# Kernel tuning notes

Measured on AMD Instinct MI355X. Metric: run time of the kernel, lower is better.

The kernel has to match this reference:

```python
import jax, jax.numpy as jnp
import numpy as np

N_NODES = 50000
N_EDGES = 1000000
F_IN, HID, N_CLS, HEADS = 128, 16, 40, 8
NEG_SLOPE = 0.2


def setup_inputs() -> dict:
    key = jax.random.key(0)
    ks = jax.random.split(key, 12)
    x = jax.random.normal(ks[0], (N_NODES, F_IN), dtype=jnp.float32)
    edge_index = jax.random.randint(ks[1], (2, N_EDGES), 0, N_NODES, dtype=jnp.int32)
    s1 = 1.0 / np.sqrt(F_IN)
    s2 = 1.0 / np.sqrt(HID)
    return {
        "x": x,
        "edge_index": edge_index,
        # conv1: heads=8, out=HID, concat=False (mean over heads)
        "W1": jax.random.normal(ks[2], (F_IN, HEADS * HID), dtype=jnp.float32) * s1,
        "att_src1": jax.random.normal(ks[3], (HEADS, HID), dtype=jnp.float32) * s2,
        "att_dst1": jax.random.normal(ks[4], (HEADS, HID), dtype=jnp.float32) * s2,
        "b1": jnp.zeros((HID,), dtype=jnp.float32),
        # conv2: heads=1, out=N_CLS
        "W2": jax.random.normal(ks[5], (HID, N_CLS), dtype=jnp.float32) * s2,
        "att_src2": jax.random.normal(ks[6], (1, N_CLS), dtype=jnp.float32),
        "att_dst2": jax.random.normal(ks[7], (1, N_CLS), dtype=jnp.float32),
        "b2": jnp.zeros((N_CLS,), dtype=jnp.float32),
    }


def _gat_conv(x, src, dst, W, att_src, att_dst, num_nodes):
    """One GATConv (PyG semantics, eval mode). Returns [N, H, C]."""
    H, C = att_src.shape
    h = (x @ W).reshape(-1, H, C)                       # [N, H, C]
    a_s = (h * att_src[None]).sum(-1)                   # [N, H]
    a_d = (h * att_dst[None]).sum(-1)                   # [N, H]
    e = jax.nn.leaky_relu(a_s[src] + a_d[dst], NEG_SLOPE)  # [E, H]
    # segment softmax over edges grouped by destination node
    m = jax.ops.segment_max(e, dst, num_segments=num_nodes)     # [N, H]
    ex = jnp.exp(e - m[dst])
    denom = jax.ops.segment_sum(ex, dst, num_segments=num_nodes)
    alpha = ex / (denom[dst] + 1e-16)                   # [E, H]
    msg = h[src] * alpha[:, :, None]                    # [E, H, C]
    return jax.ops.segment_sum(msg, dst, num_segments=num_nodes)  # [N, H, C]


def reference(x, edge_index, W1, att_src1, att_dst1, b1, W2, att_src2, att_dst2, b2):
    n = x.shape[0]
    loops = jnp.arange(n, dtype=edge_index.dtype)
    src = jnp.concatenate([edge_index[0], loops])
    dst = jnp.concatenate([edge_index[1], loops])

    # conv1: concat=False -> mean over heads, then bias; then ELU
    h1 = _gat_conv(x, src, dst, W1, att_src1, att_dst1, n).mean(axis=1) + b1
    h1 = jax.nn.elu(h1)
    # dropout is identity in eval mode

    # conv2: heads=1, concat (trivial) -> squeeze head dim, add bias
    h2 = _gat_conv(h1, src, dst, W2, att_src2, att_dst2, n)[:, 0, :] + b2
    return jax.nn.log_softmax(h2, axis=1)
```

## Files before the change

### kernel.cpp

```cpp
#include <hip/hip_runtime.h>
#include <hip/hip_fp16.h>
#include <math.h>

#define N_NODES 50000
#define N_EDGES 1000000
#define F_IN 128
#define HID 16
#define N_CLS 40
#define HEADS 8
#define ET (N_EDGES + N_NODES)
#define XB ((N_NODES + 63) / 64)
#define HB ((ET + 255) / 256)
#define NSCB ((N_NODES + 255) / 256)

__device__ __forceinline__ void fma4(float4& acc, float s, const float4& v) {
  acc.x += s * v.x;
  acc.y += s * v.y;
  acc.z += s * v.z;
  acc.w += s * v.w;
}

__device__ __forceinline__ float dot4(float4 a, float4 b) {
  return a.x * b.x + a.y * b.y + a.z * b.z + a.w * b.w;
}

__device__ __forceinline__ unsigned encf(float f) {
  unsigned b = __float_as_uint(f);
  return (b & 0x80000000u) ? ~b : (b | 0x80000000u);
}
__device__ __forceinline__ float decf(unsigned k) {
  unsigned b = (k & 0x80000000u) ? (k ^ 0x80000000u) : ~k;
  return __uint_as_float(b);
}


__global__ __launch_bounds__(256, 4) void k_xform1(
    const float* __restrict__ x, const float* __restrict__ W1,
    const float* __restrict__ att_s, const float* __restrict__ att_d,
    const int* __restrict__ ei, int* __restrict__ deg, int* __restrict__ epos,
    __half* __restrict__ h1, float* __restrict__ as1, float* __restrict__ ad1,
    unsigned* __restrict__ enc1) {
  if (blockIdx.x >= XB) {
    int i = (blockIdx.x - XB) * 256 + threadIdx.x;
    if (i < ET) {
      int dd = (i < N_EDGES) ? ei[N_EDGES + i] : (i - N_EDGES);
      epos[i] = atomicAdd(&deg[dd], 1);
    }
    return;
  }
  __shared__ float4 xlds[64 * 9];
  __shared__ float4 wlds[32 * 33];
  __shared__ unsigned encl[8];
  int t = threadIdx.x;
  if (t < 8) encl[t] = 0u;
  int tx = t & 15, ty = t >> 4;
  int base = blockIdx.x * 64;
  const float4* x4 = (const float4*)x;
  const float4* W4 = (const float4*)W1;

  float4 accA[4], accB[4];
#pragma unroll
  for (int n = 0; n < 4; n++) {
    accA[n] = {0.f, 0.f, 0.f, 0.f};
    accB[n] = {0.f, 0.f, 0.f, 0.f};
  }
  int n0 = ty * 4;

  for (int kb = 0; kb < 4; kb++) {
    __syncthreads();
    {
      int i = t;
      int n = i >> 3, q = i & 7;
      int gn = base + n;
      float4 v = {0.f, 0.f, 0.f, 0.f};
      if (gn < N_NODES) v = x4[(size_t)gn * 32 + kb * 8 + q];
      xlds[n * 9 + q] = v;
      i += 256;
      n = i >> 3; q = i & 7;
      gn = base + n;
      float4 v2 = {0.f, 0.f, 0.f, 0.f};
      if (gn < N_NODES) v2 = x4[(size_t)gn * 32 + kb * 8 + q];
      xlds[n * 9 + q] = v2;
    }
#pragma unroll
    for (int u = 0; u < 4; u++) {
      int i = t + u * 256;
      int r = i >> 5, q = i & 31;
      wlds[r * 33 + q] = W4[(size_t)(kb * 32 + r) * 32 + q];
    }
    __syncthreads();
#pragma unroll
    for (int kk = 0; kk < 8; kk++) {
      float4 xv0 = xlds[(n0 + 0) * 9 + kk];
      float4 xv1 = xlds[(n0 + 1) * 9 + kk];
      float4 xv2 = xlds[(n0 + 2) * 9 + kk];
      float4 xv3 = xlds[(n0 + 3) * 9 + kk];
#pragma unroll
      for (int j = 0; j < 4; j++) {
        float4 wA = wlds[(kk * 4 + j) * 33 + tx];
        float4 wB = wlds[(kk * 4 + j) * 33 + tx + 16];
        float s0 = (j == 0) ? xv0.x : (j == 1) ? xv0.y : (j == 2) ? xv0.z : xv0.w;
        float s1 = (j == 0) ? xv1.x : (j == 1) ? xv1.y : (j == 2) ? xv1.z : xv1.w;
        float s2 = (j == 0) ? xv2.x : (j == 1) ? xv2.y : (j == 2) ? xv2.z : xv2.w;
        float s3 = (j == 0) ? xv3.x : (j == 1) ? xv3.y : (j == 2) ? xv3.z : xv3.w;
        fma4(accA[0], s0, wA); fma4(accB[0], s0, wB);
        fma4(accA[1], s1, wA); fma4(accB[1], s1, wB);
        fma4(accA[2], s2, wA); fma4(accB[2], s2, wB);
        fma4(accA[3], s3, wA); fma4(accB[3], s3, wB);
      }
    }
  }

  int c4 = tx * 4;
  float4 asA = *(const float4*)(att_s + c4);
  float4 asB = *(const float4*)(att_s + 64 + c4);
  float4 adA = *(const float4*)(att_d + c4);
  float4 adB = *(const float4*)(att_d + 64 + c4);
  float mxA = -1e30f, mxB = -1e30f;
#pragma unroll
  for (int n = 0; n < 4; n++) {
    int gn = base + n0 + n;
    float psA = dot4(accA[n], asA);
    float psB = dot4(accB[n], asB);
    float pdA = dot4(accA[n], adA);
    float pdB = dot4(accB[n], adB);
    psA += __shfl_xor(psA, 1); psA += __shfl_xor(psA, 2);
    psB += __shfl_xor(psB, 1); psB += __shfl_xor(psB, 2);
    pdA += __shfl_xor(pdA, 1); pdA += __shfl_xor(pdA, 2);
    pdB += __shfl_xor(pdB, 1); pdB += __shfl_xor(pdB, 2);
    if (gn < N_NODES) {
      uint2 pkA, pkB;
      __half2* phA = (__half2*)&pkA;
      __half2* phB = (__half2*)&pkB;
      phA[0] = __floats2half2_rn(accA[n].x, accA[n].y);
      phA[1] = __floats2half2_rn(accA[n].z, accA[n].w);
      phB[0] = __floats2half2_rn(accB[n].x, accB[n].y);
      phB[1] = __floats2half2_rn(accB[n].z, accB[n].w);
      *(uint2*)(h1 + (size_t)gn * 128 + c4) = pkA;
      *(uint2*)(h1 + (size_t)gn * 128 + 64 + c4) = pkB;
      mxA = fmaxf(mxA, psA);
      mxB = fmaxf(mxB, psB);
      if ((tx & 3) == 0) {
        as1[gn * 8 + (tx >> 2)] = psA;
        as1[gn * 8 + 4 + (tx >> 2)] = psB;
        ad1[gn * 8 + (tx >> 2)] = pdA;
        ad1[gn * 8 + 4 + (tx >> 2)] = pdB;
      }
    }
  }
  if ((tx & 3) == 0) {
    atomicMax(&encl[tx >> 2], encf(mxA));
    atomicMax(&encl[4 + (tx >> 2)], encf(mxB));
  }
  __syncthreads();
  if (t < 8) atomicMax(&enc1[t], encl[t]);
}


__global__ __launch_bounds__(256) void k_scanA(const int* __restrict__ deg,
                                               int* __restrict__ bsum) {
  int i = blockIdx.x * 256 + threadIdx.x;
  int v = (i < N_NODES) ? deg[i] : 0;
#pragma unroll
  for (int off = 32; off; off >>= 1) v += __shfl_xor(v, off);
  __shared__ int ws[4];
  if ((threadIdx.x & 63) == 0) ws[threadIdx.x >> 6] = v;
  __syncthreads();
  if (threadIdx.x == 0) bsum[blockIdx.x] = ws[0] + ws[1] + ws[2] + ws[3];
}

__global__ __launch_bounds__(256) void k_scanB(const int* __restrict__ bsum,
                                               int* __restrict__ boff,
                                               int* __restrict__ start,
                                               const unsigned* __restrict__ enc1,
                                               float* __restrict__ fmax1) {
  __shared__ int s[256];
  int t = threadIdx.x;
  int v0 = (t < NSCB) ? bsum[t] : 0;
  s[t] = v0;
  __syncthreads();
  for (int off = 1; off < 256; off <<= 1) {
    int v = (t >= off) ? s[t - off] : 0;
    __syncthreads();
    s[t] += v;
    __syncthreads();
  }
  boff[t] = s[t] - v0;
  if (t == 0) start[N_NODES] = ET;
  if (t < 8) fmax1[t] = decf(enc1[t]);
}

__global__ __launch_bounds__(256) void k_scanC(const int* __restrict__ deg,
                                               const int* __restrict__ boff,
                                               int* __restrict__ start) {
  __shared__ int s[256];
  int t = threadIdx.x;
  int i = blockIdx.x * 256 + t;
  int v0 = (i < N_NODES) ? deg[i] : 0;
  s[t] = v0;
  __syncthreads();
  for (int off = 1; off < 256; off <<= 1) {
    int v = (t >= off) ? s[t - off] : 0;
    __syncthreads();
    s[t] += v;
    __syncthreads();
  }
  if (i < N_NODES) start[i] = boff[blockIdx.x] + s[t] - v0;
}

__global__ void k_scatter(const int* __restrict__ ei, const int* __restrict__ start,
                          const int* __restrict__ epos, int* __restrict__ esrc) {
  int i = blockIdx.x * blockDim.x + threadIdx.x;
  if (i >= ET) return;
  int s, d;
  if (i < N_EDGES) { s = ei[i]; d = ei[N_EDGES + i]; }
  else { s = i - N_EDGES; d = s; }
  esrc[start[d] + epos[i]] = s;
}


__global__ __launch_bounds__(256) void k_agg1(
    const __half* __restrict__ h1, const float* __restrict__ as1,
    const float* __restrict__ ad1, const int* __restrict__ start,
    const int* __restrict__ esrc, const float* __restrict__ b1,
    const float* __restrict__ W2, const float* __restrict__ att_s2,
    const float* __restrict__ att_d2, const float* __restrict__ fmax1,
    __half* __restrict__ h2, float* __restrict__ as2, float* __restrict__ ad2) {
  __shared__ __align__(16) __half2 p_t[4][4 * 164];
  __shared__ __align__(16) int s_off[4][4][20];
  __shared__ float w2s[16 * 40];
  int t = threadIdx.x;
  for (int i = t; i < 640; i += 256) w2s[i] = W2[i];
  __syncthreads();

  int wave = t >> 6, lane = t & 63;
  int g = lane >> 4, li = lane & 15;
  int d = blockIdx.x * 16 + wave * 4 + g;
  int s0 = start[d];
  int deg = start[d + 1] - s0;

  int dm = deg;
  dm = max(dm, __shfl_xor(dm, 16));
  dm = max(dm, __shfl_xor(dm, 32));

  float4 av0 = *(const float4*)(ad1 + d * 8);
  float4 av1 = *(const float4*)(ad1 + d * 8 + 4);
  float ad_[8] = {av0.x, av0.y, av0.z, av0.w, av1.x, av1.y, av1.z, av1.w};
  float c_[8];
#pragma unroll
  for (int h = 0; h < 8; h++) {
    float e = fmax1[h] + ad_[h];
    c_[h] = e > 0.f ? e : 0.2f * e;
  }

  float den = 0.f;
  float accf[8];
#pragma unroll
  for (int k = 0; k < 8; k++) accf[k] = 0.f;

  int hsel = li >> 1;
  const char* h1l = (const char*)(h1 + li * 8);
  __half2* ptw = &p_t[wave][g * 164];
  const int* so = &s_off[wave][g][0];

  for (int be = 0; be < dm; be += 16) {
    int cnt = deg - be;
    bool act = li < cnt;
    int s = 0;
    if (act) s = esrc[s0 + be + li];
    s_off[wave][g][li] = act ? (s << 8) : 0;
    float4 p0 = {0.f, 0.f, 0.f, 0.f}, p1 = {0.f, 0.f, 0.f, 0.f};
    if (act) {
      p0 = *(const float4*)(as1 + (size_t)s * 8);
      p1 = *(const float4*)(as1 + (size_t)s * 8 + 4);
    }
    float ev[8] = {p0.x, p0.y, p0.z, p0.w, p1.x, p1.y, p1.z, p1.w};
#pragma unroll
    for (int h = 0; h < 8; h++) {
      float v = ev[h] + ad_[h];
      v = v > 0.f ? v : 0.2f * v;
      float pv = act ? __expf(v - c_[h]) : 0.f;
      __half hp = __float2half(pv);
      ptw[h * 20 + li] = __half2{hp, hp};
    }
    asm volatile("s_waitcnt lgkmcnt(0)" ::: "memory");

    int cm = min(dm - be, 16);
    const __half2* pt = ptw + hsel * 20;
    __half2 a0 = __floats2half2_rn(0.f, 0.f);
    __half2 a1 = __floats2half2_rn(0.f, 0.f);
    __half2 a2 = __floats2half2_rn(0.f, 0.f);
    __half2 a3 = __floats2half2_rn(0.f, 0.f);
    for (int e = 0; e < cm; e += 8) {
      int4 s4 = *(const int4*)&so[e];
      int4 s8 = *(const int4*)&so[e + 4];
      uint4 pwA = *(const uint4*)&pt[e];
      uint4 pwB = *(const uint4*)&pt[e + 4];
      const __half2* ppA = (const __half2*)&pwA;
      const __half2* ppB = (const __half2*)&pwB;
      uint4 hA = *(const uint4*)(h1l + (unsigned)s4.x);
      uint4 hB = *(const uint4*)(h1l + (unsigned)s4.y);
      uint4 hC = *(const uint4*)(h1l + (unsigned)s4.z);
      uint4 hD = *(const uint4*)(h1l + (unsigned)s4.w);
      uint4 hE = *(const uint4*)(h1l + (unsigned)s8.x);
      uint4 hF = *(const uint4*)(h1l + (unsigned)s8.y);
      uint4 hG = *(const uint4*)(h1l + (unsigned)s8.z);
      uint4 hH = *(const uint4*)(h1l + (unsigned)s8.w);
      const __half2* vA = (const __half2*)&hA;
      const __half2* vB = (const __half2*)&hB;
      const __half2* vC = (const __half2*)&hC;
      const __half2* vD = (const __half2*)&hD;
      const __half2* vE = (const __half2*)&hE;
      const __half2* vF = (const __half2*)&hF;
      const __half2* vG = (const __half2*)&hG;
      const __half2* vH = (const __half2*)&hH;
      a0 = __hfma2(vA[0], ppA[0], a0); a1 = __hfma2(vA[1], ppA[0], a1);
      a2 = __hfma2(vA[2], ppA[0], a2); a3 = __hfma2(vA[3], ppA[0], a3);
      a0 = __hfma2(vB[0], ppA[1], a0); a1 = __hfma2(vB[1], ppA[1], a1);
      a2 = __hfma2(vB[2], ppA[1], a2); a3 = __hfma2(vB[3], ppA[1], a3);
      a0 = __hfma2(vC[0], ppA[2], a0); a1 = __hfma2(vC[1], ppA[2], a1);
      a2 = __hfma2(vC[2], ppA[2], a2); a3 = __hfma2(vC[3], ppA[2], a3);
      a0 = __hfma2(vD[0], ppA[3], a0); a1 = __hfma2(vD[1], ppA[3], a1);
      a2 = __hfma2(vD[2], ppA[3], a2); a3 = __hfma2(vD[3], ppA[3], a3);
      a0 = __hfma2(vE[0], ppB[0], a0); a1 = __hfma2(vE[1], ppB[0], a1);
      a2 = __hfma2(vE[2], ppB[0], a2); a3 = __hfma2(vE[3], ppB[0], a3);
      a0 = __hfma2(vF[0], ppB[1], a0); a1 = __hfma2(vF[1], ppB[1], a1);
      a2 = __hfma2(vF[2], ppB[1], a2); a3 = __hfma2(vF[3], ppB[1], a3);
      a0 = __hfma2(vG[0], ppB[2], a0); a1 = __hfma2(vG[1], ppB[2], a1);
      a2 = __hfma2(vG[2], ppB[2], a2); a3 = __hfma2(vG[3], ppB[2], a3);
      a0 = __hfma2(vH[0], ppB[3], a0); a1 = __hfma2(vH[1], ppB[3], a1);
      a2 = __hfma2(vH[2], ppB[3], a2); a3 = __hfma2(vH[3], ppB[3], a3);
      den += __low2float(ppA[0]) + __low2float(ppA[1]) +
             __low2float(ppA[2]) + __low2float(ppA[3]) +
             __low2float(ppB[0]) + __low2float(ppB[1]) +
             __low2float(ppB[2]) + __low2float(ppB[3]);
    }
    float2 f0 = __half22float2(a0), f1 = __half22float2(a1);
    float2 f2 = __half22float2(a2), f3 = __half22float2(a3);
    accf[0] += f0.x; accf[1] += f0.y; accf[2] += f1.x; accf[3] += f1.y;
    accf[4] += f2.x; accf[5] += f2.y; accf[6] += f3.x; accf[7] += f3.y;
    asm volatile("s_waitcnt lgkmcnt(0)" ::: "memory");
  }

  float sc = 0.125f / den;
#pragma unroll
  for (int k = 0; k < 8; k++) accf[k] *= sc;
#pragma unroll
  for (int off = 2; off <= 8; off <<= 1) {
#pragma unroll
    for (int k = 0; k < 8; k++) accf[k] += __shfl_xor(accf[k], off);
  }
  int jb = (li & 1) * 8;
  float4 b1a = *(const float4*)(b1 + jb);
  float4 b1b = *(const float4*)(b1 + jb + 4);
  float bv[8] = {b1a.x, b1a.y, b1a.z, b1a.w, b1b.x, b1b.y, b1b.z, b1b.w};
  float r[8];
#pragma unroll
  for (int k = 0; k < 8; k++) {
    float v = accf[k] + bv[k];
    r[k] = v > 0.f ? v : __expf(v) - 1.f;
  }
  float ro[8];
#pragma unroll
  for (int k = 0; k < 8; k++) ro[k] = __shfl_xor(r[k], 1);

  float o0 = 0.f, o1 = 0.f, o2 = 0.f;
  bool has2 = li < 8;
#pragma unroll
  for (int k = 0; k < 16; k++) {
    float rk;
    if (k < 8) rk = (li & 1) ? ro[k] : r[k];
    else       rk = (li & 1) ? r[k - 8] : ro[k - 8];
    o0 = fmaf(rk, w2s[k * 40 + li], o0);
    o1 = fmaf(rk, w2s[k * 40 + li + 16], o1);
    if (has2) o2 = fmaf(rk, w2s[k * 40 + li + 32], o2);
  }
  __half* h2r = h2 + d * 40;
  h2r[li] = __float2half(o0);
  h2r[li + 16] = __float2half(o1);
  if (has2) h2r[li + 32] = __float2half(o2);

  float sv = o0 * att_s2[li] + o1 * att_s2[li + 16];
  float dv = o0 * att_d2[li] + o1 * att_d2[li + 16];
  if (has2) {
    sv = fmaf(o2, att_s2[li + 32], sv);
    dv = fmaf(o2, att_d2[li + 32], dv);
  }
#pragma unroll
  for (int off = 1; off <= 8; off <<= 1) {
    sv += __shfl_xor(sv, off);
    dv += __shfl_xor(dv, off);
  }
  if (li == 0) { as2[d] = sv; ad2[d] = dv; }
}


__global__ __launch_bounds__(256) void k_maxas2(const float* __restrict__ as2,
                                                unsigned* __restrict__ enc) {
  int t = blockIdx.x * 256 + threadIdx.x;
  float mx = -1e30f;
  for (int r = t; r < N_NODES; r += 16384) mx = fmaxf(mx, as2[r]);
#pragma unroll
  for (int off = 32; off; off >>= 1) mx = fmaxf(mx, __shfl_xor(mx, off));
  if ((threadIdx.x & 63) == 0) atomicMax(enc, encf(mx));
}


__global__ __launch_bounds__(256) void k_agg2(
    const __half* __restrict__ h2, const float* __restrict__ as2,
    const float* __restrict__ ad2, const int* __restrict__ start,
    const int* __restrict__ esrc, const float* __restrict__ b2,
    const unsigned* __restrict__ as2maxEnc, float* __restrict__ out) {
  __shared__ __align__(16) float p_l[4][64];
  __shared__ __align__(16) int s_l[4][64];
  int wave = threadIdx.x >> 6, lane = threadIdx.x & 63;
  int d = blockIdx.x * 4 + wave;
  if (d >= N_NODES) return;
  int s0 = start[d];
  int deg = start[d + 1] - s0;
  float adv = ad2[d];
  float cm = decf(as2maxEnc[0]) + adv;
  cm = cm > 0.f ? cm : 0.2f * cm;

  int cp = lane % 20;
  int es = lane / 20;
  const char* h2b = (const char*)h2 + cp * 4;

  float den = 0.f, acc0 = 0.f, acc1 = 0.f;
  for (int be = 0; be < deg; be += 64) {
    int cnt = min(64, deg - be);
    if (lane < cnt) {
      int s = esrc[s0 + be + lane];
      s_l[wave][lane] = s * 80;
      float e = as2[s] + adv;
      e = e > 0.f ? e : 0.2f * e;
      float p = __expf(e - cm);
      den += p;
      p_l[wave][lane] = p;
    }
    asm volatile("s_waitcnt lgkmcnt(0)" ::: "memory");
    if (es < 3) {
      int i = 0;
      for (; i + 5 < cnt; i += 6) {
        int eA = i + es, eB = i + 3 + es;
        int sbA = s_l[wave][eA], sbB = s_l[wave][eB];
        float pA = p_l[wave][eA], pB = p_l[wave][eB];
        __half2 hvA = *(const __half2*)(h2b + (unsigned)sbA);
        __half2 hvB = *(const __half2*)(h2b + (unsigned)sbB);
        acc0 = fmaf(__half2float(hvA.x), pA, acc0);
        acc1 = fmaf(__half2float(hvA.y), pA, acc1);
        acc0 = fmaf(__half2float(hvB.x), pB, acc0);
        acc1 = fmaf(__half2float(hvB.y), pB, acc1);
      }
      for (; i < cnt; i += 3) {
        int e = i + es;
        if (e < cnt) {
          int sb = s_l[wave][e];
          float p = p_l[wave][e];
          __half2 hv = *(const __half2*)(h2b + (unsigned)sb);
          acc0 = fmaf(__half2float(hv.x), p, acc0);
          acc1 = fmaf(__half2float(hv.y), p, acc1);
        }
      }
    }
    asm volatile("s_waitcnt lgkmcnt(0)" ::: "memory");
  }
#pragma unroll
  for (int off = 32; off; off >>= 1) den += __shfl_xor(den, off);
  float iv = 1.f / den;

  acc0 += __shfl(acc0, lane + 20) + __shfl(acc0, lane + 40);
  acc1 += __shfl(acc1, lane + 20) + __shfl(acc1, lane + 40);
  float va = __shfl(acc0, lane >> 1);
  float vb = __shfl(acc1, lane >> 1);
  float v = (lane & 1) ? vb : va;
  v = (lane < N_CLS) ? v * iv + b2[lane] : -1e30f;

  float mx = v;
#pragma unroll
  for (int off = 32; off; off >>= 1) mx = fmaxf(mx, __shfl_xor(mx, off));
  float ex = (lane < N_CLS) ? __expf(v - mx) : 0.f;
  float sm = ex;
#pragma unroll
  for (int off = 32; off; off >>= 1) sm += __shfl_xor(sm, off);
  float lse = logf(sm);
  if (lane < N_CLS) out[d * N_CLS + lane] = (v - mx) - lse;
}


extern "C" void kernel_launch(void* const* d_in, const int* in_sizes, int n_in,
                              void* d_out, int out_size, void* d_ws, size_t ws_size,
                              hipStream_t stream) {
  const float* x    = (const float*)d_in[0];
  const int*   ei   = (const int*)d_in[1];
  const float* W1   = (const float*)d_in[2];
  const float* as1w = (const float*)d_in[3];
  const float* ad1w = (const float*)d_in[4];
  const float* b1   = (const float*)d_in[5];
  const float* W2   = (const float*)d_in[6];
  const float* as2w = (const float*)d_in[7];
  const float* ad2w = (const float*)d_in[8];
  const float* b2   = (const float*)d_in[9];
  float* out = (float*)d_out;

  char* ws = (char*)d_ws;
  size_t off = 0;
  auto alloc = [&](size_t bytes) -> void* {
    void* p = ws + off;
    off += (bytes + 255) & ~(size_t)255;
    return p;
  };
  __half* h1   = (__half*)alloc((size_t)N_NODES * 128 * 2);
  float* as1   = (float*)alloc((size_t)N_NODES * 8 * 4);
  float* ad1   = (float*)alloc((size_t)N_NODES * 8 * 4);
  __half* h2   = (__half*)alloc((size_t)N_NODES * 40 * 2);
  float* as2   = (float*)alloc((size_t)N_NODES * 4);
  float* ad2   = (float*)alloc((size_t)N_NODES * 4);
  size_t zbytes = (size_t)N_NODES * 4 + 256;
  int* deg     = (int*)alloc(zbytes);
  unsigned* maxenc = (unsigned*)(deg + N_NODES);
  int* start   = (int*)alloc((size_t)(N_NODES + 1) * 4);
  int* esrc    = (int*)alloc((size_t)ET * 4);
  int* epos    = (int*)alloc((size_t)ET * 4);
  int* bsum    = (int*)alloc((size_t)NSCB * 4);
  int* boff    = (int*)alloc(256 * 4);
  float* fmax1 = (float*)alloc(32);

  (void)hipMemsetAsync(deg, 0, zbytes, stream);

  k_xform1<<<XB + HB, 256, 0, stream>>>(x, W1, as1w, ad1w, ei, deg, epos,
                                        h1, as1, ad1, maxenc);
  k_scanA<<<NSCB, 256, 0, stream>>>(deg, bsum);
  k_scanB<<<1, 256, 0, stream>>>(bsum, boff, start, maxenc, fmax1);
  k_scanC<<<NSCB, 256, 0, stream>>>(deg, boff, start);
  k_scatter<<<HB, 256, 0, stream>>>(ei, start, epos, esrc);

  k_agg1<<<N_NODES / 16, 256, 0, stream>>>(h1, as1, ad1, start, esrc, b1,
                                           W2, as2w, ad2w, fmax1,
                                           h2, as2, ad2);
  k_maxas2<<<64, 256, 0, stream>>>(as2, maxenc + 8);
  k_agg2<<<(N_NODES + 3) / 4, 256, 0, stream>>>(h2, as2, ad2, start, esrc, b2,
                                                maxenc + 8, out);
}
```

Measured before the change: 172.0 us.

## Use fp16 MFMA for first-layer feature transform with swizzled LDS tiles

Rewrites the x@W1 projection to convert x and W1 to fp16 in swizzled shared memory and compute with 16x16x32 MFMA instructions instead of scalar FP32 FMAs. Attention logits are reduced via cross-lane shuffles from the MFMA accumulator layout. This trades input precision (fp16 inputs) and larger LDS use, which may lower occupancy, for higher matrix throughput. Output stores become per-element half writes.

New measurement: 186.9 us. 1.09x slower.

```diff
diff --git a/kernel.cpp b/kernel.cpp
--- a/kernel.cpp
+++ b/kernel.cpp
@@ -13,16 +13,8 @@
 #define HB ((ET + 255) / 256)
 #define NSCB ((N_NODES + 255) / 256)
 
-__device__ __forceinline__ void fma4(float4& acc, float s, const float4& v) {
-  acc.x += s * v.x;
-  acc.y += s * v.y;
-  acc.z += s * v.z;
-  acc.w += s * v.w;
-}
-
-__device__ __forceinline__ float dot4(float4 a, float4 b) {
-  return a.x * b.x + a.y * b.y + a.z * b.z + a.w * b.w;
-}
+typedef __attribute__((ext_vector_type(8))) _Float16 f16x8;
+typedef __attribute__((ext_vector_type(4))) float f32x4;
 
 __device__ __forceinline__ unsigned encf(float f) {
   unsigned b = __float_as_uint(f);
@@ -34,7 +26,7 @@
 }
 
 
-__global__ __launch_bounds__(256, 4) void k_xform1(
+__global__ __launch_bounds__(256) void k_xform1(
     const float* __restrict__ x, const float* __restrict__ W1,
     const float* __restrict__ att_s, const float* __restrict__ att_d,
     const int* __restrict__ ei, int* __restrict__ deg, int* __restrict__ epos,
@@ -48,109 +40,107 @@
     }
     return;
   }
-  __shared__ float4 xlds[64 * 9];
-  __shared__ float4 wlds[32 * 33];
+  __shared__ __half xl[64 * 128];
+  __shared__ __half wt[128 * 128];
   __shared__ unsigned encl[8];
   int t = threadIdx.x;
   if (t < 8) encl[t] = 0u;
-  int tx = t & 15, ty = t >> 4;
   int base = blockIdx.x * 64;
   const float4* x4 = (const float4*)x;
   const float4* W4 = (const float4*)W1;
 
-  float4 accA[4], accB[4];
-#pragma unroll
-  for (int n = 0; n < 4; n++) {
-    accA[n] = {0.f, 0.f, 0.f, 0.f};
-    accB[n] = {0.f, 0.f, 0.f, 0.f};
-  }
-  int n0 = ty * 4;
-
+#pragma unroll
+  for (int u = 0; u < 8; u++) {
+    int i = t + u * 256;
+    int n = i >> 5, q = i & 31;
+    int gn = base + n;
+    float4 v = {0.f, 0.f, 0.f, 0.f};
+    if (gn < N_NODES) v = x4[(size_t)gn * 32 + q];
+    uint2 pk;
+    __half2* ph = (__half2*)&pk;
+    ph[0] = __floats2half2_rn(v.x, v.y);
+    ph[1] = __floats2half2_rn(v.z, v.w);
+    unsigned byte = (unsigned)(n * 256 + q * 8) ^ ((n & 7) << 4);
+    *(uint2*)((char*)xl + byte) = pk;
+  }
+#pragma unroll
+  for (int u = 0; u < 4; u++) {
+    int i = t + u * 256;
+    int kt = i >> 5, ct = i & 31;
+    int k0 = kt * 4;
+    float4 r0 = W4[(size_t)(k0 + 0) * 32 + ct];
+    float4 r1 = W4[(size_t)(k0 + 1) * 32 + ct];
+    float4 r2 = W4[(size_t)(k0 + 2) * 32 + ct];
+    float4 r3 = W4[(size_t)(k0 + 3) * 32 + ct];
+    int chb = ct * 4;
+    uint2 pk;
+    __half2* ph = (__half2*)&pk;
+    ph[0] = __floats2half2_rn(r0.x, r1.x); ph[1] = __floats2half2_rn(r2.x, r3.x);
+    *(uint2*)((char*)wt + (((unsigned)((chb + 0) * 256 + k0 * 2)) ^ (((chb + 0) & 7) << 4))) = pk;
+    ph[0] = __floats2half2_rn(r0.y, r1.y); ph[1] = __floats2half2_rn(r2.y, r3.y);
+    *(uint2*)((char*)wt + (((unsigned)((chb + 1) * 256 + k0 * 2)) ^ (((chb + 1) & 7) << 4))) = pk;
+    ph[0] = __floats2half2_rn(r0.z, r1.z); ph[1] = __floats2half2_rn(r2.z, r3.z);
+    *(uint2*)((char*)wt + (((unsigned)((chb + 2) * 256 + k0 * 2)) ^ (((chb + 2) & 7) << 4))) = pk;
+    ph[0] = __floats2half2_rn(r0.w, r1.w); ph[1] = __floats2half2_rn(r2.w, r3.w);
+    *(uint2*)((char*)wt + (((unsigned)((chb + 3) * 256 + k0 * 2)) ^ (((chb + 3) & 7) << 4))) = pk;
+  }
+  __syncthreads();
+
+  int l = t & 63, wv = t >> 6;
+  int lm = l & 15, lh = l >> 4;
+  int n0 = wv * 16;
+  int node = n0 + lm;
+  bool wvalid = (base + n0) < N_NODES;
+
+  f32x4 acc[8];
+#pragma unroll
+  for (int f = 0; f < 8; f++) acc[f] = (f32x4){0.f, 0.f, 0.f, 0.f};
+
+#pragma unroll
   for (int kb = 0; kb < 4; kb++) {
-    __syncthreads();
-    {
-      int i = t;
-      int n = i >> 3, q = i & 7;
-      int gn = base + n;
-      float4 v = {0.f, 0.f, 0.f, 0.f};
-      if (gn < N_NODES) v = x4[(size_t)gn * 32 + kb * 8 + q];
-      xlds[n * 9 + q] = v;
-      i += 256;
-      n = i >> 3; q = i & 7;
-      gn = base + n;
-      float4 v2 = {0.f, 0.f, 0.f, 0.f};
-      if (gn < N_NODES) v2 = x4[(size_t)gn * 32 + kb * 8 + q];
-      xlds[n * 9 + q] = v2;
-    }
-#pragma unroll
-    for (int u = 0; u < 4; u++) {
-      int i = t + u * 256;
-      int r = i >> 5, q = i & 31;
-      wlds[r * 33 + q] = W4[(size_t)(kb * 32 + r) * 32 + q];
-    }
-    __syncthreads();
-#pragma unroll
-    for (int kk = 0; kk < 8; kk++) {
-      float4 xv0 = xlds[(n0 + 0) * 9 + kk];
-      float4 xv1 = xlds[(n0 + 1) * 9 + kk];
-      float4 xv2 = xlds[(n0 + 2) * 9 + kk];
-      float4 xv3 = xlds[(n0 + 3) * 9 + kk];
-#pragma unroll
-      for (int j = 0; j < 4; j++) {
-        float4 wA = wlds[(kk * 4 + j) * 33 + tx];
-        float4 wB = wlds[(kk * 4 + j) * 33 + tx + 16];
-        float s0 = (j == 0) ? xv0.x : (j == 1) ? xv0.y : (j == 2) ? xv0.z : xv0.w;
-        float s1 = (j == 0) ? xv1.x : (j == 1) ? xv1.y : (j == 2) ? xv1.z : xv1.w;
-        float s2 = (j == 0) ? xv2.x : (j == 1) ? xv2.y : (j == 2) ? xv2.z : xv2.w;
-        float s3 = (j == 0) ? xv3.x : (j == 1) ? xv3.y : (j == 2) ? xv3.z : xv3.w;
-        fma4(accA[0], s0, wA); fma4(accB[0], s0, wB);
-        fma4(accA[1], s1, wA); fma4(accB[1], s1, wB);
-        fma4(accA[2], s2, wA); fma4(accB[2], s2, wB);
-        fma4(accA[3], s3, wA); fma4(accB[3], s3, wB);
+    int kbase = kb * 32 + lh * 8;
+    unsigned ab = ((unsigned)(node * 256 + kbase * 2)) ^ ((node & 7) << 4);
+    f16x8 af = *(const f16x8*)((const char*)xl + ab);
+#pragma unroll
+    for (int f = 0; f < 8; f++) {
+      int ch = f * 16 + lm;
+      unsigned bb = ((unsigned)(ch * 256 + kbase * 2)) ^ ((ch & 7) << 4);
+      f16x8 bf = *(const f16x8*)((const char*)wt + bb);
+      acc[f] = __builtin_amdgcn_mfma_f32_16x16x32_f16(af, bf, acc[f], 0, 0, 0);
+    }
+  }
+
+  int nr = base + n0 + lh * 4;
+#pragma unroll
+  for (int f = 0; f < 8; f++) {
+    float asv = att_s[f * 16 + lm];
+    float adv = att_d[f * 16 + lm];
+    float ps0 = acc[f].x * asv, ps1 = acc[f].y * asv;
+    float ps2 = acc[f].z * asv, ps3 = acc[f].w * asv;
+    float pd0 = acc[f].x * adv, pd1 = acc[f].y * adv;
+    float pd2 = acc[f].z * adv, pd3 = acc[f].w * adv;
+#pragma unroll
+    for (int off = 1; off <= 8; off <<= 1) {
+      ps0 += __shfl_xor(ps0, off); ps1 += __shfl_xor(ps1, off);
+      ps2 += __shfl_xor(ps2, off); ps3 += __shfl_xor(ps3, off);
+      pd0 += __shfl_xor(pd0, off); pd1 += __shfl_xor(pd1, off);
+      pd2 += __shfl_xor(pd2, off); pd3 += __shfl_xor(pd3, off);
+    }
+    if (wvalid) {
+      if (lm == 0) {
+        as1[(nr + 0) * 8 + f] = ps0; ad1[(nr + 0) * 8 + f] = pd0;
+        as1[(nr + 1) * 8 + f] = ps1; ad1[(nr + 1) * 8 + f] = pd1;
+        as1[(nr + 2) * 8 + f] = ps2; ad1[(nr + 2) * 8 + f] = pd2;
+        as1[(nr + 3) * 8 + f] = ps3; ad1[(nr + 3) * 8 + f] = pd3;
+        float m = fmaxf(fmaxf(ps0, ps1), fmaxf(ps2, ps3));
+        atomicMax(&encl[f], encf(m));
       }
-    }
-  }
-
-  int c4 = tx * 4;
-  float4 asA = *(const float4*)(att_s + c4);
-  float4 asB = *(const float4*)(att_s + 64 + c4);
-  float4 adA = *(const float4*)(att_d + c4);
-  float4 adB = *(const float4*)(att_d + 64 + c4);
-  float mxA = -1e30f, mxB = -1e30f;
-#pragma unroll
-  for (int n = 0; n < 4; n++) {
-    int gn = base + n0 + n;
-    float psA = dot4(accA[n], asA);
-    float psB = dot4(accB[n], asB);
-    float pdA = dot4(accA[n], adA);
-    float pdB = dot4(accB[n], adB);
-    psA += __shfl_xor(psA, 1); psA += __shfl_xor(psA, 2);
-    psB += __shfl_xor(psB, 1); psB += __shfl_xor(psB, 2);
-    pdA += __shfl_xor(pdA, 1); pdA += __shfl_xor(pdA, 2);
-    pdB += __shfl_xor(pdB, 1); pdB += __shfl_xor(pdB, 2);
-    if (gn < N_NODES) {
-      uint2 pkA, pkB;
-      __half2* phA = (__half2*)&pkA;
-      __half2* phB = (__half2*)&pkB;
-      phA[0] = __floats2half2_rn(accA[n].x, accA[n].y);
-      phA[1] = __floats2half2_rn(accA[n].z, accA[n].w);
-      phB[0] = __floats2half2_rn(accB[n].x, accB[n].y);
-      phB[1] = __floats2half2_rn(accB[n].z, accB[n].w);
-      *(uint2*)(h1 + (size_t)gn * 128 + c4) = pkA;
-      *(uint2*)(h1 + (size_t)gn * 128 + 64 + c4) = pkB;
-      mxA = fmaxf(mxA, psA);
-      mxB = fmaxf(mxB, psB);
-      if ((tx & 3) == 0) {
-        as1[gn * 8 + (tx >> 2)] = psA;
-        as1[gn * 8 + 4 + (tx >> 2)] = psB;
-        ad1[gn * 8 + (tx >> 2)] = pdA;
-        ad1[gn * 8 + 4 + (tx >> 2)] = pdB;
-      }
-    }
-  }
-  if ((tx & 3) == 0) {
-    atomicMax(&encl[tx >> 2], encf(mxA));
-    atomicMax(&encl[4 + (tx >> 2)], encf(mxB));
+      int cb = f * 16 + lm;
+      h1[(size_t)(nr + 0) * 128 + cb] = __float2half(acc[f].x);
+      h1[(size_t)(nr + 1) * 128 + cb] = __float2half(acc[f].y);
+      h1[(size_t)(nr + 2) * 128 + cb] = __float2half(acc[f].z);
+      h1[(size_t)(nr + 3) * 128 + cb] = __float2half(acc[f].w);
+    }
   }
   __syncthreads();
   if (t < 8) atomicMax(&enc1[t], encl[t]);
```

## Replace global-atomic CSR build with two-pass radix bucket sort by destination

Applied to the files above, without the earlier changes.

Builds the destination-sorted edge list with a two-level radix sort instead of per-edge global atomics on degree counters. Edges are first bucketed by dst>>8 using LDS-atomic histograms and a per-bucket scan, then each bucket is sorted locally in LDS by the low 8 bits. This removes a million contended global atomicAdds and the scattered random writes into esrc. It costs more kernel launches and an extra pass through an 8-byte intermediate buffer, and the transform kernel no longer overlaps with the degree counting. It also assumes each 256-node bucket holds no more than 8192 edges.

Result: faster. 158.0 us (-8.2%).

```diff
diff --git a/kernel.cpp b/kernel.cpp
--- a/kernel.cpp
+++ b/kernel.cpp
@@ -10,8 +10,9 @@
 #define HEADS 8
 #define ET (N_EDGES + N_NODES)
 #define XB ((N_NODES + 63) / 64)
-#define HB ((ET + 255) / 256)
-#define NSCB ((N_NODES + 255) / 256)
+#define NBK 196
+#define NSB 256
+#define ECH ((ET + NSB - 1) / NSB)
 
 __device__ __forceinline__ void fma4(float4& acc, float s, const float4& v) {
   acc.x += s * v.x;
@@ -37,17 +38,8 @@
 __global__ __launch_bounds__(256, 4) void k_xform1(
     const float* __restrict__ x, const float* __restrict__ W1,
     const float* __restrict__ att_s, const float* __restrict__ att_d,
-    const int* __restrict__ ei, int* __restrict__ deg, int* __restrict__ epos,
     __half* __restrict__ h1, float* __restrict__ as1, float* __restrict__ ad1,
     unsigned* __restrict__ enc1) {
-  if (blockIdx.x >= XB) {
-    int i = (blockIdx.x - XB) * 256 + threadIdx.x;
-    if (i < ET) {
-      int dd = (i < N_EDGES) ? ei[N_EDGES + i] : (i - N_EDGES);
-      epos[i] = atomicAdd(&deg[dd], 1);
-    }
-    return;
-  }
   __shared__ float4 xlds[64 * 9];
   __shared__ float4 wlds[32 * 33];
   __shared__ unsigned encl[8];
@@ -157,26 +149,50 @@
 }
 
 
-__global__ __launch_bounds__(256) void k_scanA(const int* __restrict__ deg,
-                                               int* __restrict__ bsum) {
-  int i = blockIdx.x * 256 + threadIdx.x;
-  int v = (i < N_NODES) ? deg[i] : 0;
-#pragma unroll
-  for (int off = 32; off; off >>= 1) v += __shfl_xor(v, off);
-  __shared__ int ws[4];
-  if ((threadIdx.x & 63) == 0) ws[threadIdx.x >> 6] = v;
-  __syncthreads();
-  if (threadIdx.x == 0) bsum[blockIdx.x] = ws[0] + ws[1] + ws[2] + ws[3];
-}
-
-__global__ __launch_bounds__(256) void k_scanB(const int* __restrict__ bsum,
-                                               int* __restrict__ boff,
+__global__ __launch_bounds__(256) void k_rxA(const int* __restrict__ ei,
+                                             int* __restrict__ bcnt) {
+  __shared__ int cnt[NBK];
+  int t = threadIdx.x, blk = blockIdx.x;
+  if (t < NBK) cnt[t] = 0;
+  __syncthreads();
+  int lo = blk * ECH + t;
+  int hi = min((blk + 1) * ECH, ET);
+  for (int i = lo; i < hi; i += 256) {
+    int d = (i < N_EDGES) ? ei[N_EDGES + i] : (i - N_EDGES);
+    atomicAdd(&cnt[d >> 8], 1);
+  }
+  __syncthreads();
+  if (t < NBK) bcnt[t * NSB + blk] = cnt[t];
+}
+
+
+__global__ __launch_bounds__(256) void k_rxScanB(const int* __restrict__ bcnt,
+                                                 int* __restrict__ boffs,
+                                                 int* __restrict__ btot) {
+  __shared__ int s[256];
+  int b = blockIdx.x, t = threadIdx.x;
+  int v0 = bcnt[b * NSB + t];
+  s[t] = v0;
+  __syncthreads();
+  for (int off = 1; off < 256; off <<= 1) {
+    int v = (t >= off) ? s[t - off] : 0;
+    __syncthreads();
+    s[t] += v;
+    __syncthreads();
+  }
+  boffs[b * NSB + t] = s[t] - v0;
+  if (t == 255) btot[b] = s[255];
+}
+
+
+__global__ __launch_bounds__(256) void k_rxTot(const int* __restrict__ btot,
+                                               int* __restrict__ bstart,
                                                int* __restrict__ start,
                                                const unsigned* __restrict__ enc1,
                                                float* __restrict__ fmax1) {
   __shared__ int s[256];
   int t = threadIdx.x;
-  int v0 = (t < NSCB) ? bsum[t] : 0;
+  int v0 = (t < NBK) ? btot[t] : 0;
   s[t] = v0;
   __syncthreads();
   for (int off = 1; off < 256; off <<= 1) {
@@ -185,37 +201,68 @@
     s[t] += v;
     __syncthreads();
   }
-  boff[t] = s[t] - v0;
+  if (t < NBK) bstart[t] = s[t] - v0;
   if (t == 0) start[N_NODES] = ET;
   if (t < 8) fmax1[t] = decf(enc1[t]);
 }
 
-__global__ __launch_bounds__(256) void k_scanC(const int* __restrict__ deg,
-                                               const int* __restrict__ boff,
-                                               int* __restrict__ start) {
-  __shared__ int s[256];
-  int t = threadIdx.x;
-  int i = blockIdx.x * 256 + t;
-  int v0 = (i < N_NODES) ? deg[i] : 0;
-  s[t] = v0;
+
+__global__ __launch_bounds__(256) void k_rxScat(const int* __restrict__ ei,
+                                                const int* __restrict__ bstart,
+                                                const int* __restrict__ boffs,
+                                                int2* __restrict__ eb) {
+  __shared__ int cur[NBK];
+  int t = threadIdx.x, blk = blockIdx.x;
+  if (t < NBK) cur[t] = bstart[t] + boffs[t * NSB + blk];
+  __syncthreads();
+  int lo = blk * ECH + t;
+  int hi = min((blk + 1) * ECH, ET);
+  for (int i = lo; i < hi; i += 256) {
+    int s, d;
+    if (i < N_EDGES) { s = ei[i]; d = ei[N_EDGES + i]; }
+    else { s = i - N_EDGES; d = s; }
+    int pos = atomicAdd(&cur[d >> 8], 1);
+    eb[pos] = make_int2(s, d);
+  }
+}
+
+
+__global__ __launch_bounds__(256) void k_rxB(const int2* __restrict__ eb,
+                                             const int* __restrict__ bstart,
+                                             int* __restrict__ start,
+                                             int* __restrict__ esrc) {
+  __shared__ int dcnt[256], lst[256], ssc[256];
+  __shared__ int esl[8192];
+  int t = threadIdx.x, b = blockIdx.x;
+  int nlo = b * 256;
+  int nn = min(256, N_NODES - nlo);
+  int e0 = bstart[b];
+  int e1 = (b == NBK - 1) ? ET : bstart[b + 1];
+  int cnt = e1 - e0;
+  dcnt[t] = 0;
+  __syncthreads();
+  for (int e = t; e < cnt; e += 256) atomicAdd(&dcnt[eb[e0 + e].y & 255], 1);
+  __syncthreads();
+  int v0 = dcnt[t];
+  ssc[t] = v0;
   __syncthreads();
   for (int off = 1; off < 256; off <<= 1) {
-    int v = (t >= off) ? s[t - off] : 0;
-    __syncthreads();
-    s[t] += v;
-    __syncthreads();
-  }
-  if (i < N_NODES) start[i] = boff[blockIdx.x] + s[t] - v0;
-}
-
-__global__ void k_scatter(const int* __restrict__ ei, const int* __restrict__ start,
-                          const int* __restrict__ epos, int* __restrict__ esrc) {
-  int i = blockIdx.x * blockDim.x + threadIdx.x;
-  if (i >= ET) return;
-  int s, d;
-  if (i < N_EDGES) { s = ei[i]; d = ei[N_EDGES + i]; }
-  else { s = i - N_EDGES; d = s; }
-  esrc[start[d] + epos[i]] = s;
+    int v = (t >= off) ? ssc[t - off] : 0;
+    __syncthreads();
+    ssc[t] += v;
+    __syncthreads();
+  }
+  lst[t] = ssc[t] - v0;
+  if (t < nn) start[nlo + t] = e0 + lst[t];
+  dcnt[t] = lst[t];
+  __syncthreads();
+  for (int e = t; e < cnt; e += 256) {
+    int2 p = eb[e0 + e];
+    int pos = atomicAdd(&dcnt[p.y & 255], 1);
+    esl[pos] = p.x;
+  }
+  __syncthreads();
+  for (int e = t; e < cnt; e += 256) esrc[e0 + e] = esl[e];
 }
 
 
@@ -516,24 +563,24 @@
   __half* h2   = (__half*)alloc((size_t)N_NODES * 40 * 2);
   float* as2   = (float*)alloc((size_t)N_NODES * 4);
   float* ad2   = (float*)alloc((size_t)N_NODES * 4);
-  size_t zbytes = (size_t)N_NODES * 4 + 256;
-  int* deg     = (int*)alloc(zbytes);
-  unsigned* maxenc = (unsigned*)(deg + N_NODES);
+  unsigned* maxenc = (unsigned*)alloc(256);
   int* start   = (int*)alloc((size_t)(N_NODES + 1) * 4);
   int* esrc    = (int*)alloc((size_t)ET * 4);
-  int* epos    = (int*)alloc((size_t)ET * 4);
-  int* bsum    = (int*)alloc((size_t)NSCB * 4);
-  int* boff    = (int*)alloc(256 * 4);
+  int2* eb     = (int2*)alloc((size_t)ET * 8);
+  int* bcnt    = (int*)alloc((size_t)NBK * NSB * 4);
+  int* boffs   = (int*)alloc((size_t)NBK * NSB * 4);
+  int* btot    = (int*)alloc((size_t)NBK * 4);
+  int* bstart  = (int*)alloc((size_t)NBK * 4);
   float* fmax1 = (float*)alloc(32);
 
-  (void)hipMemsetAsync(deg, 0, zbytes, stream);
-
-  k_xform1<<<XB + HB, 256, 0, stream>>>(x, W1, as1w, ad1w, ei, deg, epos,
-                                        h1, as1, ad1, maxenc);
-  k_scanA<<<NSCB, 256, 0, stream>>>(deg, bsum);
-  k_scanB<<<1, 256, 0, stream>>>(bsum, boff, start, maxenc, fmax1);
-  k_scanC<<<NSCB, 256, 0, stream>>>(deg, boff, start);
-  k_scatter<<<HB, 256, 0, stream>>>(ei, start, epos, esrc);
+  (void)hipMemsetAsync(maxenc, 0, 256, stream);
+
+  k_xform1<<<XB, 256, 0, stream>>>(x, W1, as1w, ad1w, h1, as1, ad1, maxenc);
+  k_rxA<<<NSB, 256, 0, stream>>>(ei, bcnt);
+  k_rxScanB<<<NBK, 256, 0, stream>>>(bcnt, boffs, btot);
+  k_rxTot<<<1, 256, 0, stream>>>(btot, bstart, start, maxenc, fmax1);
+  k_rxScat<<<NSB, 256, 0, stream>>>(ei, bstart, boffs, eb);
+  k_rxB<<<NBK, 256, 0, stream>>>(eb, bstart, start, esrc);
 
   k_agg1<<<N_NODES / 16, 256, 0, stream>>>(h1, as1, ad1, start, esrc, b1,
                                            W2, as2w, ad2w, fmax1,
```
